# Kernel optimization log

Measured on AMD Instinct MI355X. Metric: run time of the kernel, lower is better.

## Reference

```python
import jax, jax.numpy as jnp
import numpy as np

# Grid config from init_kwargs
VX, VY = 0.1, 0.1
XMIN, YMIN, ZMIN, XMAX, YMAX, ZMAX = 0.0, -25.6, -3.0, 51.2, 25.6, 3.0
H = int(round((XMAX - XMIN) / VX))  # 512
W = int(round((YMAX - YMIN) / VY))  # 512
SIGMA = 1.5   # gaussian std in voxel units
R = 3         # splat window radius -> 7x7 kernel


def _pose0to1(pose0, pose1):
    # ego-motion: pose1^{-1} @ pose0, per batch element
    return jnp.linalg.inv(pose1) @ pose0


def _transform(xyz, pose):
    # xyz: [B,N,3], pose: [B,4,4] -> xyz @ R^T + t
    Rm = pose[:, :3, :3]
    t = pose[:, :3, 3]
    return jnp.einsum('bnd,bed->bne', xyz, Rm) + t[:, None, :]


def _voxelize(xyz):
    # continuous voxel coords + integer pillar indices + in-range mask
    px = (xyz[..., 0] - XMIN) / VX
    py = (xyz[..., 1] - YMIN) / VY
    ix = jnp.floor(px).astype(jnp.int32)
    iy = jnp.floor(py).astype(jnp.int32)
    valid = (ix >= 0) & (ix < H) & (iy >= 0) & (iy < W) & \
            (xyz[..., 2] >= ZMIN) & (xyz[..., 2] < ZMAX)
    return px, py, ix, iy, valid


def _gauss_heatmap(px, py, ix, iy, valid):
    # Splat a gaussian (max-composited) around every valid radar pillar.
    B, M = px.shape
    offs = jnp.arange(-R, R + 1)
    dx, dy = jnp.meshgrid(offs, offs, indexing='ij')      # [K,K]
    gx = ix[:, :, None, None] + dx                        # [B,M,K,K]
    gy = iy[:, :, None, None] + dy
    cellx = gx.astype(px.dtype) + 0.5
    celly = gy.astype(py.dtype) + 0.5
    d2 = (cellx - px[:, :, None, None]) ** 2 + (celly - py[:, :, None, None]) ** 2
    val = jnp.exp(-d2 / (2.0 * SIGMA * SIGMA))
    inb = (gx >= 0) & (gx < H) & (gy >= 0) & (gy < W) & valid[:, :, None, None]
    bidx = jnp.arange(B, dtype=jnp.int32)[:, None, None, None]
    flat = jnp.where(inb, bidx * (H * W) + gx * W + gy, B * H * W)  # dummy seg for invalid
    heat = jax.ops.segment_max(val.reshape(-1), flat.reshape(-1),
                               num_segments=B * H * W + 1)
    heat = jnp.maximum(heat[:B * H * W], 0.0).reshape(B, H, W)
    return heat


def _gather(heat, ix, iy, valid):
    # per-point gaussian score = heatmap at the point's pillar
    B = heat.shape[0]
    hf = heat.reshape(B, -1)
    idx = jnp.clip(ix, 0, H - 1) * W + jnp.clip(iy, 0, W - 1)
    s = jnp.take_along_axis(hf, idx, axis=1)
    return jnp.where(valid, s, 0.0)


def _forward(pc0, pc1, radar_pc0, radar_pc1, pose0, pose1):
    # pose computed under no_grad in the original -> stop_gradient
    pose_0to1 = jax.lax.stop_gradient(_pose0to1(pose0, pose1))
    tpc0 = _transform(pc0, pose_0to1)
    trad0_xyz = _transform(radar_pc0[..., :3], pose_0to1)
    # dynamic pillar voxelization (BEV coords)
    _, _, l0x, l0y, l0v = _voxelize(tpc0)
    _, _, l1x, l1y, l1v = _voxelize(pc1)
    r0px, r0py, r0x, r0y, r0v = _voxelize(trad0_xyz)
    r1px, r1py, r1x, r1y, r1v = _voxelize(radar_pc1[..., :3])
    # gaussian maps from radar pillars, scored for lidar + radar points
    heat0 = _gauss_heatmap(r0px, r0py, r0x, r0y, r0v)
    heat1 = _gauss_heatmap(r1px, r1py, r1x, r1y, r1v)
    lidar0 = _gather(heat0, l0x, l0y, l0v)   # [B,N]
    radar0 = _gather(heat0, r0x, r0y, r0v)   # [B,M]
    lidar1 = _gather(heat1, l1x, l1y, l1v)
    radar1 = _gather(heat1, r1x, r1y, r1v)
    return jnp.concatenate([lidar0, radar0, lidar1, radar1], axis=1)


def setup_inputs() -> dict:
    key = jax.random.key(0)
    ks = jax.random.split(key, 8)
    B, N, M = 8, 262144, 8192
    lo = jnp.array([XMIN, YMIN, ZMIN], dtype=jnp.float32)
    hi = jnp.array([XMAX, YMAX, ZMAX], dtype=jnp.float32)
    pc0 = jax.random.uniform(ks[0], (B, N, 3), dtype=jnp.float32) * (hi - lo) + lo
    pc1 = jax.random.uniform(ks[1], (B, N, 3), dtype=jnp.float32) * (hi - lo) + lo
    rxyz0 = jax.random.uniform(ks[2], (B, M, 3), dtype=jnp.float32) * (hi - lo) + lo
    rxyz1 = jax.random.uniform(ks[3], (B, M, 3), dtype=jnp.float32) * (hi - lo) + lo
    radar_pc0 = jnp.concatenate([rxyz0, jax.random.normal(ks[4], (B, M, 3), dtype=jnp.float32)], axis=-1)
    radar_pc1 = jnp.concatenate([rxyz1, jax.random.normal(ks[5], (B, M, 3), dtype=jnp.float32)], axis=-1)

    def mk_pose(k):
        t = jax.random.uniform(k, (B, 3), minval=-0.5, maxval=0.5, dtype=jnp.float32)
        eye = jnp.tile(jnp.eye(4, dtype=jnp.float32)[None], (B, 1, 1))
        return eye.at[:, :3, 3].set(t)

    pose0 = mk_pose(ks[6])
    pose1 = mk_pose(ks[7])
    return {"pc0": pc0, "pc1": pc1, "radar_pc0": radar_pc0,
            "radar_pc1": radar_pc1, "pose0": pose0, "pose1": pose1}


def reference(pc0, pc1, radar_pc0, radar_pc1, pose0, pose1):
    return _forward(pc0, pc1, radar_pc0, radar_pc1, pose0, pose1)
```

## Files before the change

### kernel.cpp

```cpp
#include <hip/hip_runtime.h>
#include <math.h>

#define GH 512
#define GW 512
#define GHW (GH * GW)
#define RR 3
#define SH 32
#define SSHIFT 5
#define NSTRIP (GH / SH)
#define SCAP 1024
#define THR 1024
#define GCHUNK 1024


__device__ __forceinline__ void compute_pose(const float* __restrict__ P0,
                                             const float* __restrict__ P1,
                                             float* __restrict__ T) {
    double a00 = P1[0], a01 = P1[1], a02 = P1[2],  t1x = P1[3];
    double a10 = P1[4], a11 = P1[5], a12 = P1[6],  t1y = P1[7];
    double a20 = P1[8], a21 = P1[9], a22 = P1[10], t1z = P1[11];
    double c00 = a11 * a22 - a12 * a21;
    double c01 = a12 * a20 - a10 * a22;
    double c02 = a10 * a21 - a11 * a20;
    double det = a00 * c00 + a01 * c01 + a02 * c02;
    double id = 1.0 / det;
    double r00 = c00 * id;
    double r01 = (a02 * a21 - a01 * a22) * id;
    double r02 = (a01 * a12 - a02 * a11) * id;
    double r10 = c01 * id;
    double r11 = (a00 * a22 - a02 * a20) * id;
    double r12 = (a02 * a10 - a00 * a12) * id;
    double r20 = c02 * id;
    double r21 = (a01 * a20 - a00 * a21) * id;
    double r22 = (a00 * a11 - a01 * a10) * id;

    double b00 = P0[0], b01 = P0[1], b02 = P0[2],  t0x = P0[3];
    double b10 = P0[4], b11 = P0[5], b12 = P0[6],  t0y = P0[7];
    double b20 = P0[8], b21 = P0[9], b22 = P0[10], t0z = P0[11];
    double dx = t0x - t1x, dy = t0y - t1y, dz = t0z - t1z;

    T[0]  = (float)(r00 * b00 + r01 * b10 + r02 * b20);
    T[1]  = (float)(r00 * b01 + r01 * b11 + r02 * b21);
    T[2]  = (float)(r00 * b02 + r01 * b12 + r02 * b22);
    T[3]  = (float)(r00 * dx + r01 * dy + r02 * dz);
    T[4]  = (float)(r10 * b00 + r11 * b10 + r12 * b20);
    T[5]  = (float)(r10 * b01 + r11 * b11 + r12 * b21);
    T[6]  = (float)(r10 * b02 + r11 * b12 + r12 * b22);
    T[7]  = (float)(r10 * dx + r11 * dy + r12 * dz);
    T[8]  = (float)(r20 * b00 + r21 * b10 + r22 * b20);
    T[9]  = (float)(r20 * b01 + r21 * b11 + r22 * b21);
    T[10] = (float)(r20 * b02 + r21 * b12 + r22 * b22);
    T[11] = (float)(r20 * dx + r21 * dy + r22 * dz);
}

__device__ __forceinline__ void voxelize_xyz(float x, float y, float z,
                                             const float* __restrict__ T,
                                             float& px, float& py,
                                             int& ix, int& iy, bool& valid) {
    if (T) {
        float nx = T[0] * x + T[1] * y + T[2] * z + T[3];
        float ny = T[4] * x + T[5] * y + T[6] * z + T[7];
        float nz = T[8] * x + T[9] * y + T[10] * z + T[11];
        x = nx; y = ny; z = nz;
    }
    px = (x - 0.0f) * 10.0f;
    py = (y - (-25.6f)) * 10.0f;
    ix = (int)floorf(px);
    iy = (int)floorf(py);
    valid = (ix >= 0) & (ix < GH) & (iy >= 0) & (iy < GW) &
            (z >= -3.0f) & (z < 3.0f);
}

__global__ __launch_bounds__(THR)
void heat_strip_kernel(const float* __restrict__ radar0,
                       const float* __restrict__ radar1,
                       const float* __restrict__ pose0,
                       const float* __restrict__ pose1,
                       float* __restrict__ heat0,
                       float* __restrict__ heat1,
                       int B, int M) {
    __shared__ int strip[SH * GW];
    __shared__ float2 sp[SCAP];
    __shared__ float Tsh[8][12];
    __shared__ int sn;

    const int tid = threadIdx.x;
    const int lane = tid & 63;
    const int blk = blockIdx.x;
    const int b = blk % B;
    const int map = (blk / B) & 1;
    const int sx = blk / (2 * B);
    const int x0 = sx << SSHIFT;

    if (tid < B) compute_pose(pose0 + tid * 16, pose1 + tid * 16, &Tsh[tid][0]);
    if (tid == 0) sn = 0;
    {
        const int4 z4 = make_int4(0, 0, 0, 0);
        for (int c4 = tid * 4; c4 < SH * GW; c4 += 4 * THR)
            *reinterpret_cast<int4*>(&strip[c4]) = z4;
    }
    __syncthreads();

    const float* radar = map ? radar1 : radar0;
    const float* pb = radar + (size_t)b * M * 6;
    const bool hasT = (map == 0);
    const float* T = &Tsh[b][0];

    const int Mceil = (M + THR - 1) / THR * THR;
    for (int i0 = 0; i0 < Mceil; i0 += THR) {
        int i = i0 + tid;
        bool valid = false;
        float px = 0.0f, py = 0.0f;
        if (i < M) {
            const float* p = pb + (size_t)i * 6;
            float x = p[0], y = p[1], z = p[2];
            float nx = hasT ? (T[0] * x + T[1] * y + T[2] * z + T[3]) : x;
            px = (nx - 0.0f) * 10.0f;
            int ix = (int)floorf(px);
            if (ix >= x0 - RR && ix <= x0 + SH - 1 + RR) {
                float ny = hasT ? (T[4] * x + T[5] * y + T[6] * z + T[7]) : y;
                float nz = hasT ? (T[8] * x + T[9] * y + T[10] * z + T[11]) : z;
                py = (ny - (-25.6f)) * 10.0f;
                int iy = (int)floorf(py);
                valid = (ix >= 0) & (ix < GH) & (iy >= 0) & (iy < GW) &
                        (nz >= -3.0f) & (nz < 3.0f);
            }
        }
        unsigned long long mask = __ballot(valid);
        if (valid) {
            int leader = __ffsll((long long)mask) - 1;
            int cnt = __popcll(mask);
            int wbase = 0;
            if (lane == leader) wbase = atomicAdd(&sn, cnt);
            wbase = __shfl(wbase, leader);
            int off = __popcll(mask & ((1ull << lane) - 1ull));
            int slot = wbase + off;
            if (slot < SCAP) sp[slot] = make_float2(px, py);
        }
    }
    __syncthreads();

    int n = sn; if (n > SCAP) n = SCAP;
    const int total = n * 49;
    for (int t = tid; t < total; t += THR) {
        int pi = t / 49;
        int c = t - pi * 49;
        float px = sp[pi].x;
        float py = sp[pi].y;
        int ix = (int)floorf(px);
        int iy = (int)floorf(py);
        int dx = c / 7 - RR;
        int dy = c - (c / 7) * 7 - RR;
        int gx = ix + dx, gy = iy + dy;
        if (gx < x0 || gx >= x0 + SH || gy < 0 || gy >= GW) continue;
        float ddx = ((float)gx + 0.5f) - px;
        float ddy = ((float)gy + 0.5f) - py;
        float d2 = ddx * ddx + ddy * ddy;
        float val = expf(-d2 / 4.5f);
        atomicMax(&strip[(gx - x0) * GW + gy], __float_as_int(val));
    }
    __syncthreads();

    float* heat = map ? heat1 : heat0;
    float* hb = heat + (size_t)b * GHW + (size_t)x0 * GW;
    for (int c4 = tid * 4; c4 < SH * GW; c4 += 4 * THR) {
        int4 iv = *reinterpret_cast<const int4*>(&strip[c4]);
        float4 fv;
        fv.x = __int_as_float(iv.x);
        fv.y = __int_as_float(iv.y);
        fv.z = __int_as_float(iv.z);
        fv.w = __int_as_float(iv.w);
        *reinterpret_cast<float4*>(hb + c4) = fv;
    }
}

__global__ __launch_bounds__(256)
void gather_fused_kernel(const float* __restrict__ pc0,
                         const float* __restrict__ pc1,
                         const float* __restrict__ radar0,
                         const float* __restrict__ radar1,
                         const float* __restrict__ pose0,
                         const float* __restrict__ pose1,
                         const float* __restrict__ heat0,
                         const float* __restrict__ heat1,
                         float* __restrict__ out,
                         int N, int M) {
    __shared__ float Tsh[12];
    const int row_len = 2 * N + 2 * M;
    const int b = blockIdx.x;
    const int base = blockIdx.y * GCHUNK + threadIdx.x;

    if (threadIdx.x == 0) compute_pose(pose0 + b * 16, pose1 + b * 16, Tsh);
    __syncthreads();

    const float* hb0 = heat0 + (size_t)b * GHW;
    const float* hb1 = heat1 + (size_t)b * GHW;
    const float* Tb = Tsh;

    float xs[4], ys[4], zs[4];
    const float* Ts[4];
    const float* hbs[4];
    bool live[4];

    #pragma unroll
    for (int k = 0; k < 4; k++) {
        int r = base + k * 256;
        live[k] = (r < row_len);
        if (!live[k]) continue;
        const float* p;
        const float* T = nullptr;
        const float* hb;
        if (r < N) {
            p = pc0 + ((size_t)b * N + r) * 3;
            T = Tb;
            hb = hb0;
        } else if (r < N + M) {
            p = radar0 + ((size_t)b * M + (r - N)) * 6;
            T = Tb;
            hb = hb0;
        } else if (r < 2 * N + M) {
            p = pc1 + ((size_t)b * N + (r - N - M)) * 3;
            hb = hb1;
        } else {
            p = radar1 + ((size_t)b * M + (r - 2 * N - M)) * 6;
            hb = hb1;
        }
        xs[k] = __builtin_nontemporal_load(p + 0);
        ys[k] = __builtin_nontemporal_load(p + 1);
        zs[k] = __builtin_nontemporal_load(p + 2);
        Ts[k] = T;
        hbs[k] = hb;
    }

    float v[4];
    #pragma unroll
    for (int k = 0; k < 4; k++) {
        if (!live[k]) continue;
        float px, py; int ix, iy; bool valid;
        voxelize_xyz(xs[k], ys[k], zs[k], Ts[k], px, py, ix, iy, valid);
        v[k] = 0.0f;
        if (valid) v[k] = hbs[k][ix * GW + iy];
    }

    #pragma unroll
    for (int k = 0; k < 4; k++) {
        if (!live[k]) continue;
        int r = base + k * 256;
        __builtin_nontemporal_store(v[k], out + (size_t)b * row_len + r);
    }
}

extern "C" void kernel_launch(void* const* d_in, const int* in_sizes, int n_in,
                              void* d_out, int out_size, void* d_ws, size_t ws_size,
                              hipStream_t stream) {
    const float* pc0      = (const float*)d_in[0];
    const float* pc1      = (const float*)d_in[1];
    const float* radar0   = (const float*)d_in[2];
    const float* radar1   = (const float*)d_in[3];
    const float* pose0    = (const float*)d_in[4];
    const float* pose1    = (const float*)d_in[5];
    float* out = (float*)d_out;

    int B = in_sizes[4] / 16;
    int N = in_sizes[0] / (B * 3);
    int M = in_sizes[2] / (B * 6);
    int row_len = 2 * N + 2 * M;

    float* heat0 = (float*)d_ws;
    float* heat1 = heat0 + (size_t)B * GHW;

    int nblk = 2 * B * NSTRIP;
    heat_strip_kernel<<<nblk, THR, 0, stream>>>(
        radar0, radar1, pose0, pose1, heat0, heat1, B, M);

    dim3 ggrid(B, (row_len + GCHUNK - 1) / GCHUNK);
    gather_fused_kernel<<<ggrid, 256, 0, stream>>>(
        pc0, pc1, radar0, radar1, pose0, pose1, heat0, heat1, out, N, M);
}
```

Measured before the change: 142.4 us.

## Vectorize radar and point loads, halve strip height, add aligned gather kernel

```diff
diff --git a/kernel.cpp b/kernel.cpp
--- a/kernel.cpp
+++ b/kernel.cpp
@@ -5,52 +5,54 @@
 #define GW 512
 #define GHW (GH * GW)
 #define RR 3
-#define SH 32
-#define SSHIFT 5
+#define SH 16
+#define SSHIFT 4
 #define NSTRIP (GH / SH)
 #define SCAP 1024
 #define THR 1024
-#define GCHUNK 1024
+#define GTHR 256
+
+typedef float f32x4 __attribute__((ext_vector_type(4)));
 
 
 __device__ __forceinline__ void compute_pose(const float* __restrict__ P0,
                                              const float* __restrict__ P1,
                                              float* __restrict__ T) {
-    double a00 = P1[0], a01 = P1[1], a02 = P1[2],  t1x = P1[3];
-    double a10 = P1[4], a11 = P1[5], a12 = P1[6],  t1y = P1[7];
-    double a20 = P1[8], a21 = P1[9], a22 = P1[10], t1z = P1[11];
-    double c00 = a11 * a22 - a12 * a21;
-    double c01 = a12 * a20 - a10 * a22;
-    double c02 = a10 * a21 - a11 * a20;
-    double det = a00 * c00 + a01 * c01 + a02 * c02;
-    double id = 1.0 / det;
-    double r00 = c00 * id;
-    double r01 = (a02 * a21 - a01 * a22) * id;
-    double r02 = (a01 * a12 - a02 * a11) * id;
-    double r10 = c01 * id;
-    double r11 = (a00 * a22 - a02 * a20) * id;
-    double r12 = (a02 * a10 - a00 * a12) * id;
-    double r20 = c02 * id;
-    double r21 = (a01 * a20 - a00 * a21) * id;
-    double r22 = (a00 * a11 - a01 * a10) * id;
-
-    double b00 = P0[0], b01 = P0[1], b02 = P0[2],  t0x = P0[3];
-    double b10 = P0[4], b11 = P0[5], b12 = P0[6],  t0y = P0[7];
-    double b20 = P0[8], b21 = P0[9], b22 = P0[10], t0z = P0[11];
-    double dx = t0x - t1x, dy = t0y - t1y, dz = t0z - t1z;
-
-    T[0]  = (float)(r00 * b00 + r01 * b10 + r02 * b20);
-    T[1]  = (float)(r00 * b01 + r01 * b11 + r02 * b21);
-    T[2]  = (float)(r00 * b02 + r01 * b12 + r02 * b22);
-    T[3]  = (float)(r00 * dx + r01 * dy + r02 * dz);
-    T[4]  = (float)(r10 * b00 + r11 * b10 + r12 * b20);
-    T[5]  = (float)(r10 * b01 + r11 * b11 + r12 * b21);
-    T[6]  = (float)(r10 * b02 + r11 * b12 + r12 * b22);
-    T[7]  = (float)(r10 * dx + r11 * dy + r12 * dz);
-    T[8]  = (float)(r20 * b00 + r21 * b10 + r22 * b20);
-    T[9]  = (float)(r20 * b01 + r21 * b11 + r22 * b21);
-    T[10] = (float)(r20 * b02 + r21 * b12 + r22 * b22);
-    T[11] = (float)(r20 * dx + r21 * dy + r22 * dz);
+    float a00 = P1[0], a01 = P1[1], a02 = P1[2],  t1x = P1[3];
+    float a10 = P1[4], a11 = P1[5], a12 = P1[6],  t1y = P1[7];
+    float a20 = P1[8], a21 = P1[9], a22 = P1[10], t1z = P1[11];
+    float c00 = a11 * a22 - a12 * a21;
+    float c01 = a12 * a20 - a10 * a22;
+    float c02 = a10 * a21 - a11 * a20;
+    float det = a00 * c00 + a01 * c01 + a02 * c02;
+    float id = 1.0f / det;
+    float r00 = c00 * id;
+    float r01 = (a02 * a21 - a01 * a22) * id;
+    float r02 = (a01 * a12 - a02 * a11) * id;
+    float r10 = c01 * id;
+    float r11 = (a00 * a22 - a02 * a20) * id;
+    float r12 = (a02 * a10 - a00 * a12) * id;
+    float r20 = c02 * id;
+    float r21 = (a01 * a20 - a00 * a21) * id;
+    float r22 = (a00 * a11 - a01 * a10) * id;
+
+    float b00 = P0[0], b01 = P0[1], b02 = P0[2],  t0x = P0[3];
+    float b10 = P0[4], b11 = P0[5], b12 = P0[6],  t0y = P0[7];
+    float b20 = P0[8], b21 = P0[9], b22 = P0[10], t0z = P0[11];
+    float dx = t0x - t1x, dy = t0y - t1y, dz = t0z - t1z;
+
+    T[0]  = r00 * b00 + r01 * b10 + r02 * b20;
+    T[1]  = r00 * b01 + r01 * b11 + r02 * b21;
+    T[2]  = r00 * b02 + r01 * b12 + r02 * b22;
+    T[3]  = r00 * dx + r01 * dy + r02 * dz;
+    T[4]  = r10 * b00 + r11 * b10 + r12 * b20;
+    T[5]  = r10 * b01 + r11 * b11 + r12 * b21;
+    T[6]  = r10 * b02 + r11 * b12 + r12 * b22;
+    T[7]  = r10 * dx + r11 * dy + r12 * dz;
+    T[8]  = r20 * b00 + r21 * b10 + r22 * b20;
+    T[9]  = r20 * b01 + r21 * b11 + r22 * b21;
+    T[10] = r20 * b02 + r21 * b12 + r22 * b22;
+    T[11] = r20 * dx + r21 * dy + r22 * dz;
 }
 
 __device__ __forceinline__ void voxelize_xyz(float x, float y, float z,
@@ -71,7 +73,7 @@
             (z >= -3.0f) & (z < 3.0f);
 }
 
-__global__ __launch_bounds__(THR)
+__global__ __launch_bounds__(THR, 8)
 void heat_strip_kernel(const float* __restrict__ radar0,
                        const float* __restrict__ radar1,
                        const float* __restrict__ pose0,
@@ -103,12 +105,57 @@
 
     const float* radar = map ? radar1 : radar0;
     const float* pb = radar + (size_t)b * M * 6;
+    const f32x4* pb4 = reinterpret_cast<const f32x4*>(pb);
     const bool hasT = (map == 0);
     const float* T = &Tsh[b][0];
 
-    const int Mceil = (M + THR - 1) / THR * THR;
-    for (int i0 = 0; i0 < Mceil; i0 += THR) {
-        int i = i0 + tid;
+    const int ng = M >> 2;
+    for (int g0 = 0; g0 < ng; g0 += THR) {
+        int g = g0 + tid;
+        bool inr = (g < ng);
+        float X[4], Y[4], Z[4];
+        if (inr) {
+            const f32x4* s = pb4 + (size_t)g * 6;
+            f32x4 q0 = s[0], q1 = s[1], q2 = s[2];
+            f32x4 q3 = s[3], q4 = s[4], q5 = s[5];
+            X[0] = q0.x; Y[0] = q0.y; Z[0] = q0.z;
+            X[1] = q1.z; Y[1] = q1.w; Z[1] = q2.x;
+            X[2] = q3.x; Y[2] = q3.y; Z[2] = q3.z;
+            X[3] = q4.z; Y[3] = q4.w; Z[3] = q5.x;
+        }
+        #pragma unroll
+        for (int j = 0; j < 4; j++) {
+            bool valid = false;
+            float px = 0.0f, py = 0.0f;
+            if (inr) {
+                float x = X[j], y = Y[j], z = Z[j];
+                float nx = hasT ? (T[0] * x + T[1] * y + T[2] * z + T[3]) : x;
+                px = (nx - 0.0f) * 10.0f;
+                int ix = (int)floorf(px);
+                if (ix >= x0 - RR && ix <= x0 + SH - 1 + RR) {
+                    float ny = hasT ? (T[4] * x + T[5] * y + T[6] * z + T[7]) : y;
+                    float nz = hasT ? (T[8] * x + T[9] * y + T[10] * z + T[11]) : z;
+                    py = (ny - (-25.6f)) * 10.0f;
+                    int iy = (int)floorf(py);
+                    valid = (ix >= 0) & (ix < GH) & (iy >= 0) & (iy < GW) &
+                            (nz >= -3.0f) & (nz < 3.0f);
+                }
+            }
+            unsigned long long mask = __ballot(valid);
+            if (valid) {
+                int leader = __ffsll((long long)mask) - 1;
+                int cnt = __popcll(mask);
+                int wbase = 0;
+                if (lane == leader) wbase = atomicAdd(&sn, cnt);
+                wbase = __shfl(wbase, leader);
+                int off = __popcll(mask & ((1ull << lane) - 1ull));
+                int slot = wbase + off;
+                if (slot < SCAP) sp[slot] = make_float2(px, py);
+            }
+        }
+    }
+    if (M & 3) {
+        int i = (M & ~3) + tid;
         bool valid = false;
         float px = 0.0f, py = 0.0f;
         if (i < M) {
@@ -174,7 +221,90 @@
     }
 }
 
-__global__ __launch_bounds__(256)
+__global__ __launch_bounds__(GTHR)
+void gather_vec_kernel(const float* __restrict__ pc0,
+                       const float* __restrict__ pc1,
+                       const float* __restrict__ radar0,
+                       const float* __restrict__ radar1,
+                       const float* __restrict__ pose0,
+                       const float* __restrict__ pose1,
+                       const float* __restrict__ heat0,
+                       const float* __restrict__ heat1,
+                       float* __restrict__ out,
+                       int N, int M) {
+    __shared__ float Tsh[12];
+    const int row_len = 2 * N + 2 * M;
+    const int b = blockIdx.x;
+
+    if (threadIdx.x == 0) compute_pose(pose0 + b * 16, pose1 + b * 16, Tsh);
+    __syncthreads();
+
+    const float* hb0 = heat0 + (size_t)b * GHW;
+    const float* hb1 = heat1 + (size_t)b * GHW;
+
+    const int ncp = N >> 10;
+    const int ncr = M >> 10;
+    const int c = blockIdx.y;
+
+    const float* segbase;
+    const float* T = nullptr;
+    const float* hb;
+    int stride, out_base, pseg;
+    if (c < ncp) {
+        segbase = pc0 + (size_t)b * N * 3; stride = 3;
+        out_base = 0;          T = Tsh; hb = hb0; pseg = c << 10;
+    } else if (c < ncp + ncr) {
+        segbase = radar0 + (size_t)b * M * 6; stride = 6;
+        out_base = N;          T = Tsh; hb = hb0; pseg = (c - ncp) << 10;
+    } else if (c < 2 * ncp + ncr) {
+        segbase = pc1 + (size_t)b * N * 3; stride = 3;
+        out_base = N + M;               hb = hb1; pseg = (c - ncp - ncr) << 10;
+    } else {
+        segbase = radar1 + (size_t)b * M * 6; stride = 6;
+        out_base = 2 * N + M;           hb = hb1; pseg = (c - 2 * ncp - ncr) << 10;
+    }
+
+    const int p0 = pseg + threadIdx.x * 4;
+    float X[4], Y[4], Z[4];
+    if (stride == 3) {
+        const f32x4* s = reinterpret_cast<const f32x4*>(segbase + (size_t)p0 * 3);
+        f32x4 f0 = __builtin_nontemporal_load(s + 0);
+        f32x4 f1 = __builtin_nontemporal_load(s + 1);
+        f32x4 f2 = __builtin_nontemporal_load(s + 2);
+        X[0] = f0.x; Y[0] = f0.y; Z[0] = f0.z;
+        X[1] = f0.w; Y[1] = f1.x; Z[1] = f1.y;
+        X[2] = f1.z; Y[2] = f1.w; Z[2] = f2.x;
+        X[3] = f2.y; Y[3] = f2.z; Z[3] = f2.w;
+    } else {
+        const f32x4* s = reinterpret_cast<const f32x4*>(segbase + (size_t)p0 * 6);
+        f32x4 g0 = __builtin_nontemporal_load(s + 0);
+        f32x4 g1 = __builtin_nontemporal_load(s + 1);
+        f32x4 g2 = __builtin_nontemporal_load(s + 2);
+        f32x4 g3 = __builtin_nontemporal_load(s + 3);
+        f32x4 g4 = __builtin_nontemporal_load(s + 4);
+        f32x4 g5 = __builtin_nontemporal_load(s + 5);
+        X[0] = g0.x; Y[0] = g0.y; Z[0] = g0.z;
+        X[1] = g1.z; Y[1] = g1.w; Z[1] = g2.x;
+        X[2] = g3.x; Y[2] = g3.y; Z[2] = g3.z;
+        X[3] = g4.z; Y[3] = g4.w; Z[3] = g5.x;
+    }
+
+    float v[4];
+    #pragma unroll
+    for (int k = 0; k < 4; k++) {
+        float px, py; int ix, iy; bool valid;
+        voxelize_xyz(X[k], Y[k], Z[k], T, px, py, ix, iy, valid);
+        v[k] = 0.0f;
+        if (valid) v[k] = hb[ix * GW + iy];
+    }
+
+    f32x4 res;
+    res.x = v[0]; res.y = v[1]; res.z = v[2]; res.w = v[3];
+    __builtin_nontemporal_store(res,
+        reinterpret_cast<f32x4*>(out + (size_t)b * row_len + out_base + p0));
+}
+
+__global__ __launch_bounds__(GTHR)
 void gather_fused_kernel(const float* __restrict__ pc0,
                          const float* __restrict__ pc1,
                          const float* __restrict__ radar0,
@@ -188,65 +318,35 @@
     __shared__ float Tsh[12];
     const int row_len = 2 * N + 2 * M;
     const int b = blockIdx.x;
-    const int base = blockIdx.y * GCHUNK + threadIdx.x;
+    const int base = blockIdx.y * 1024 + threadIdx.x;
 
     if (threadIdx.x == 0) compute_pose(pose0 + b * 16, pose1 + b * 16, Tsh);
     __syncthreads();
 
     const float* hb0 = heat0 + (size_t)b * GHW;
     const float* hb1 = heat1 + (size_t)b * GHW;
-    const float* Tb = Tsh;
-
-    float xs[4], ys[4], zs[4];
-    const float* Ts[4];
-    const float* hbs[4];
-    bool live[4];
 
     #pragma unroll
     for (int k = 0; k < 4; k++) {
-        int r = base + k * 256;
-        live[k] = (r < row_len);
-        if (!live[k]) continue;
+        int r = base + k * GTHR;
+        if (r >= row_len) continue;
         const float* p;
         const float* T = nullptr;
         const float* hb;
         if (r < N) {
-            p = pc0 + ((size_t)b * N + r) * 3;
-            T = Tb;
-            hb = hb0;
+            p = pc0 + ((size_t)b * N + r) * 3; T = Tsh; hb = hb0;
         } else if (r < N + M) {
-            p = radar0 + ((size_t)b * M + (r - N)) * 6;
-            T = Tb;
-            hb = hb0;
+            p = radar0 + ((size_t)b * M + (r - N)) * 6; T = Tsh; hb = hb0;
         } else if (r < 2 * N + M) {
-            p = pc1 + ((size_t)b * N + (r - N - M)) * 3;
-            hb = hb1;
+            p = pc1 + ((size_t)b * N + (r - N - M)) * 3; hb = hb1;
         } else {
-            p = radar1 + ((size_t)b * M + (r - 2 * N - M)) * 6;
-            hb = hb1;
-        }
-        xs[k] = __builtin_nontemporal_load(p + 0);
-        ys[k] = __builtin_nontemporal_load(p + 1);
-        zs[k] = __builtin_nontemporal_load(p + 2);
-        Ts[k] = T;
-        hbs[k] = hb;
-    }
-
-    float v[4];
-    #pragma unroll
-    for (int k = 0; k < 4; k++) {
-        if (!live[k]) continue;
+            p = radar1 + ((size_t)b * M + (r - 2 * N - M)) * 6; hb = hb1;
+        }
         float px, py; int ix, iy; bool valid;
-        voxelize_xyz(xs[k], ys[k], zs[k], Ts[k], px, py, ix, iy, valid);
-        v[k] = 0.0f;
-        if (valid) v[k] = hbs[k][ix * GW + iy];
-    }
-
-    #pragma unroll
-    for (int k = 0; k < 4; k++) {
-        if (!live[k]) continue;
-        int r = base + k * 256;
-        __builtin_nontemporal_store(v[k], out + (size_t)b * row_len + r);
+        voxelize_xyz(p[0], p[1], p[2], T, px, py, ix, iy, valid);
+        float v = 0.0f;
+        if (valid) v = hb[ix * GW + iy];
+        __builtin_nontemporal_store(v, out + (size_t)b * row_len + r);
     }
 }
 
@@ -273,7 +373,13 @@
     heat_strip_kernel<<<nblk, THR, 0, stream>>>(
         radar0, radar1, pose0, pose1, heat0, heat1, B, M);
 
-    dim3 ggrid(B, (row_len + GCHUNK - 1) / GCHUNK);
-    gather_fused_kernel<<<ggrid, 256, 0, stream>>>(
-        pc0, pc1, radar0, radar1, pose0, pose1, heat0, heat1, out, N, M);
-}
+    if (((N & 1023) == 0) && ((M & 1023) == 0)) {
+        dim3 ggrid(B, 2 * (N >> 10) + 2 * (M >> 10));
+        gather_vec_kernel<<<ggrid, GTHR, 0, stream>>>(
+            pc0, pc1, radar0, radar1, pose0, pose1, heat0, heat1, out, N, M);
+    } else {
+        dim3 ggrid(B, (row_len + 1023) / 1024);
+        gather_fused_kernel<<<ggrid, GTHR, 0, stream>>>(
+            pc0, pc1, radar0, radar1, pose0, pose1, heat0, heat1, out, N, M);
+    }
+}
```

Result: slower. 148.3 us (+4.2%).
